# Optimization experiments

Measured on AMD Instinct MI355X. Metric: run time of the kernel, lower is better.

Reference implementation:

```python
import jax, jax.numpy as jnp
import numpy as np


def conv2d(x, w, b, stride, pad):
    # x: NCHW, w: OIHW (torch layout)
    y = jax.lax.conv_general_dilated(
        x, w, (stride, stride), ((pad, pad), (pad, pad)),
        dimension_numbers=('NCHW', 'OIHW', 'NCHW'))
    return y + b[None, :, None, None]


def conv_transpose2d(x, w, b, stride, pad):
    # w: torch ConvTranspose2d layout [in, out, kH, kW]
    k = w.shape[2]
    w_t = jnp.flip(w, (2, 3)).transpose(1, 0, 2, 3)  # -> OIHW
    p = k - 1 - pad
    y = jax.lax.conv_general_dilated(
        x, w_t, (1, 1), ((p, p), (p, p)), lhs_dilation=(stride, stride),
        dimension_numbers=('NCHW', 'OIHW', 'NCHW'))
    return y + b[None, :, None, None]


def resblock(x, w1, b1, w2, b2):
    h = jax.nn.relu(x)
    h = conv2d(h, w1, b1, 1, 1)   # 3x3
    h = jax.nn.relu(h)
    h = conv2d(h, w2, b2, 1, 0)   # 1x1
    return x + h


def setup_inputs() -> dict:
    key = jax.random.key(0)
    ks = iter(jax.random.split(key, 32))
    K, D = 512, 256
    s = 0.05

    def rn(shape):
        return (jax.random.normal(next(ks), shape, dtype=jnp.float32) * s)

    inp = {
        'x': jax.random.uniform(next(ks), (32, 3, 128, 128), dtype=jnp.float32),
        'e_c1_w': rn((256, 3, 4, 4)),   'e_c1_b': jnp.zeros((256,), jnp.float32),
        'e_c2_w': rn((256, 256, 4, 4)), 'e_c2_b': jnp.zeros((256,), jnp.float32),
        'e_r1_w1': rn((256, 256, 3, 3)), 'e_r1_b1': jnp.zeros((256,), jnp.float32),
        'e_r1_w2': rn((256, 256, 1, 1)), 'e_r1_b2': jnp.zeros((256,), jnp.float32),
        'e_r2_w1': rn((256, 256, 3, 3)), 'e_r2_b1': jnp.zeros((256,), jnp.float32),
        'e_r2_w2': rn((256, 256, 1, 1)), 'e_r2_b2': jnp.zeros((256,), jnp.float32),
        'emb': jax.random.normal(next(ks), (K, D), dtype=jnp.float32) / K,
        'd_r1_w1': rn((256, 256, 3, 3)), 'd_r1_b1': jnp.zeros((256,), jnp.float32),
        'd_r1_w2': rn((256, 256, 1, 1)), 'd_r1_b2': jnp.zeros((256,), jnp.float32),
        'd_r2_w1': rn((256, 256, 3, 3)), 'd_r2_b1': jnp.zeros((256,), jnp.float32),
        'd_r2_w2': rn((256, 256, 1, 1)), 'd_r2_b2': jnp.zeros((256,), jnp.float32),
        'd_t1_w': rn((256, 256, 4, 4)), 'd_t1_b': jnp.zeros((256,), jnp.float32),
        'd_t2_w': rn((256, 3, 4, 4)),   'd_t2_b': jnp.zeros((3,), jnp.float32),
    }
    return inp


def reference(x, e_c1_w, e_c1_b, e_c2_w, e_c2_b,
              e_r1_w1, e_r1_b1, e_r1_w2, e_r1_b2,
              e_r2_w1, e_r2_b1, e_r2_w2, e_r2_b2,
              emb,
              d_r1_w1, d_r1_b1, d_r1_w2, d_r1_b2,
              d_r2_w1, d_r2_b1, d_r2_w2, d_r2_b2,
              d_t1_w, d_t1_b, d_t2_w, d_t2_b):
    # ---- encoder ----
    h = jax.nn.relu(conv2d(x, e_c1_w, e_c1_b, 2, 1))
    h = jax.nn.relu(conv2d(h, e_c2_w, e_c2_b, 2, 1))
    h = resblock(h, e_r1_w1, e_r1_b1, e_r1_w2, e_r1_b2)
    z_e_x = resblock(h, e_r2_w1, e_r2_b1, e_r2_w2, e_r2_b2)  # [B,256,h,w]

    # ---- VQ: fused squared-distance + argmin (same math as
    # sum((z - e)^2, -2).argmin(-1), without the (B,h,w,256,K) intermediate) ----
    z = z_e_x.transpose(0, 2, 3, 1)                      # [B,h,w,256]
    z2 = jnp.sum(z * z, axis=-1, keepdims=True)          # [B,h,w,1]
    e2 = jnp.sum(emb * emb, axis=-1)                     # [K]
    dists = z2 - 2.0 * jnp.einsum('bhwd,kd->bhwk', z, emb) + e2
    latents = jnp.argmin(dists, axis=-1)                 # [B,h,w] int

    # ---- decoder ----
    z_q = emb[latents]                                   # [B,h,w,256]
    z_q_x = z_q.transpose(0, 3, 1, 2)                    # [B,256,h,w]
    d = resblock(z_q_x, d_r1_w1, d_r1_b1, d_r1_w2, d_r1_b2)
    d = resblock(d, d_r2_w1, d_r2_b1, d_r2_w2, d_r2_b2)
    d = jax.nn.relu(conv_transpose2d(d, d_t1_w, d_t1_b, 2, 1))
    x_tilde = jax.nn.sigmoid(conv_transpose2d(d, d_t2_w, d_t2_b, 2, 1))
    return x_tilde, z_e_x, z_q_x
```

## Files before the change

kernel.cpp:

```cpp
#include <hip/hip_runtime.h>
#include <math.h>

using frag_ab = __attribute__((ext_vector_type(8))) short;
using f32x4   = __attribute__((ext_vector_type(4))) float;

__device__ __forceinline__ unsigned short f2b(float f) {
    unsigned u = __float_as_uint(f);
    u += 0x7fffu + ((u >> 16) & 1u);
    return (unsigned short)(u >> 16);
}
__device__ __forceinline__ void bf8_to_f(uint4 v, float* f) {
    const unsigned* p = (const unsigned*)&v;
    #pragma unroll
    for (int q = 0; q < 4; ++q) {
        unsigned u = p[q];
        f[2*q]   = __uint_as_float(u << 16);
        f[2*q+1] = __uint_as_float(u & 0xffff0000u);
    }
}
__device__ __forceinline__ void gload16(const void* g, void* l) {
    __builtin_amdgcn_global_load_lds(g, l, 16, 0, 0);
}

__global__ void k_wt(const float* __restrict__ in, unsigned short* __restrict__ out,
                     int total, int CO, int CI, int sO, int sI) {
    int i = blockIdx.x * 256 + threadIdx.x;
    if (i >= total) return;
    int ci = i % CI;
    int r  = i / CI;
    int co = r % CO;
    int tp = r / CO;
    out[i] = f2b(in[(size_t)co * sO + (size_t)ci * sI + tp]);
}
__global__ void k_wt16(const float* __restrict__ in, unsigned short* __restrict__ out,
                       int sO, int sI) {
    int i = blockIdx.x * 256 + threadIdx.x;
    int ci = i & 255, co = i >> 8;
    const float* p = in + (size_t)co * sO + (size_t)ci * sI;
    #pragma unroll
    for (int tp = 0; tp < 16; ++tp)
        out[tp * 65536 + i] = f2b(p[tp]);
}
__global__ void k_wt3(const float* p0, const float* p1, const float* p2, const float* p3,
                      unsigned short* o0, unsigned short* o1, unsigned short* o2,
                      unsigned short* o3) {
    int z = blockIdx.y;
    const float* in = (z == 0) ? p0 : (z == 1) ? p1 : (z == 2) ? p2 : p3;
    unsigned short* out = (z == 0) ? o0 : (z == 1) ? o1 : (z == 2) ? o2 : o3;
    int i = blockIdx.x * 256 + threadIdx.x;
    int ci = i & 255, co = i >> 8;
    const float* p = in + (size_t)co * 2304 + (size_t)ci * 9;
    #pragma unroll
    for (int tp = 0; tp < 9; ++tp)
        out[tp * 65536 + i] = f2b(p[tp]);
}
__global__ void k_wt1(const float* p0, const float* p1, const float* p2, const float* p3,
                      unsigned short* o0, unsigned short* o1, unsigned short* o2,
                      unsigned short* o3) {
    int z = blockIdx.y;
    const float* in = (z == 0) ? p0 : (z == 1) ? p1 : (z == 2) ? p2 : p3;
    unsigned short* out = (z == 0) ? o0 : (z == 1) ? o1 : (z == 2) ? o2 : o3;
    int i = blockIdx.x * 256 + threadIdx.x;
    int ci = i & 255, co = i >> 8;
    out[i] = f2b(in[co * 256 + ci]);
}
__global__ void k_embcast(const float* __restrict__ in, unsigned short* __restrict__ out) {
    int i = blockIdx.x * 256 + threadIdx.x;
    out[i] = f2b(in[i]);
}

__global__ void k_e2(const float* __restrict__ emb, float* __restrict__ e2,
                     float* __restrict__ zpad) {
    if (blockIdx.x == 2) { zpad[threadIdx.x] = 0.f; return; }
    int k = blockIdx.x * 256 + threadIdx.x;
    if (k < 512) {
        const float* r = emb + k * 256;
        float s = 0.f;
        #pragma unroll 8
        for (int d = 0; d < 256; ++d) s += r[d] * r[d];
        e2[k] = s;
    }
}

__global__ __launch_bounds__(256) void k_conv1(const float* __restrict__ x,
        const float* __restrict__ w, const float* __restrict__ bias,
        unsigned short* __restrict__ out) {
    int t = threadIdx.x;
    int y = blockIdx.x * 4 + (t >> 6);
    int xq = t & 63;
    int b = blockIdx.y;
    int co0 = blockIdx.z * 64;
    float patch[48];
    #pragma unroll
    for (int ci = 0; ci < 3; ++ci)
        #pragma unroll
        for (int ky = 0; ky < 4; ++ky)
            #pragma unroll
            for (int kx = 0; kx < 4; ++kx) {
                int sy = 2*y - 1 + ky, sx = 2*xq - 1 + kx;
                float v = 0.f;
                if ((unsigned)sy < 128u && (unsigned)sx < 128u)
                    v = x[((b*3 + ci)*128 + sy)*128 + sx];
                patch[(ci*4 + ky)*4 + kx] = v;
            }
    unsigned short* op = out + (((size_t)(b*64 + y)*64 + xq) << 8) + co0;
    for (int c8 = 0; c8 < 8; ++c8) {
        unsigned short u8[8];
        #pragma unroll
        for (int cc = 0; cc < 8; ++cc) {
            int co = co0 + c8*8 + cc;
            float a = bias[co];
            #pragma unroll
            for (int k = 0; k < 48; ++k) a = fmaf(w[co*48 + k], patch[k], a);
            u8[cc] = f2b(fmaxf(a, 0.f));
        }
        *(uint4*)(op + c8*8) = *(uint4*)u8;
    }
}

template<int MODE, bool RELU_OUT, bool RELU_B16>
__global__ __launch_bounds__(256) void k_cgemm(
        const unsigned short* __restrict__ A,
        const unsigned short* __restrict__ Wt,
        const float* __restrict__ bias,
        const float* __restrict__ skipF,
        const unsigned short* __restrict__ zpad,
        unsigned short* __restrict__ outB,
        float* __restrict__ outFn,
        float* __restrict__ outFc) {
    constexpr int NTAPS = (MODE==0) ? 16 : (MODE==1) ? 9 : (MODE==2) ? 1 : 4;
    constexpr int HIN   = (MODE==0) ? 64 : 32;
    constexpr bool ISCT   = (MODE==3);

    __shared__ __align__(16) unsigned short As[128*128];
    __shared__ __align__(16) unsigned short Bs[128*128];

    int t = threadIdx.x;
    int cob = blockIdx.x;
    int y0  = blockIdx.y * 4;
    int bz  = blockIdx.z;
    int b   = ISCT ? (bz >> 2) : bz;
    int par = ISCT ? (bz & 3) : 0;
    int psy = par >> 1, psx = par & 1;

    int scc = t & 15, sr0 = t >> 4;
    int sc2 = scc ^ (sr0 & 7);

    int wv = t >> 6, lane = t & 63;
    int mq = (wv >> 1) * 64, nq = (wv & 1) * 64;
    int lg = lane >> 4, lr = lane & 15;

    f32x4 acc[4][4];
    #pragma unroll
    for (int i = 0; i < 4; ++i)
        #pragma unroll
        for (int j = 0; j < 4; ++j) acc[i][j] = (f32x4){0.f,0.f,0.f,0.f};

    for (int tap = 0; tap < NTAPS; ++tap) {
        int tdy, tdx, wtap;
        if (MODE == 0)      { tdy = tap >> 2; tdx = tap & 3; wtap = tap; }
        else if (MODE == 1) { tdy = tap / 3;  tdx = tap % 3; wtap = tap; }
        else if (MODE == 2) { tdy = 0; tdx = 0; wtap = 0; }
        else { int jy = tap >> 1, jx = tap & 1;
               tdy = psy - jy; tdx = psx - jx;
               wtap = ((psy ? 0 : 1) + 2*jy) * 4 + ((psx ? 0 : 1) + 2*jx); }
        const unsigned short* wb = Wt + ((size_t)wtap << 16) + ((size_t)cob << 15);

        for (int half = 0; half < 2; ++half) {
            int kk0 = half * 128;
            __syncthreads();
            #pragma unroll
            for (int q = 0; q < 8; ++q) {
                int row = sr0 + 16*q;
                int soy = y0 + (row >> 5), sox = row & 31;
                int sy = (MODE == 0) ? (2*soy - 1 + tdy)
                       : (MODE == 1) ? (soy - 1 + tdy) : (soy + tdy);
                int sx = (MODE == 0) ? (2*sox - 1 + tdx)
                       : (MODE == 1) ? (sox - 1 + tdx) : (sox + tdx);
                bool val = ((unsigned)sy < (unsigned)HIN) && ((unsigned)sx < (unsigned)HIN);
                const unsigned short* asrc = val
                    ? A + ((((size_t)(b*HIN + sy))*HIN + sx) << 8) + kk0 + sc2*8
                    : zpad;
                gload16(asrc, (char*)As + q*4096 + t*16);
                gload16(wb + (((size_t)row) << 8) + kk0 + sc2*8,
                        (char*)Bs + q*4096 + t*16);
            }
            __syncthreads();
            #pragma unroll
            for (int ks = 0; ks < 4; ++ks) {
                int c = ks*4 + lg;
                frag_ab af[4], bf[4];
                #pragma unroll
                for (int i = 0; i < 4; ++i) {
                    int ar = mq + i*16 + lr;
                    af[i] = *(const frag_ab*)((const char*)As + ar*256 + ((c ^ (ar & 7)) << 4));
                    int br = nq + i*16 + lr;
                    bf[i] = *(const frag_ab*)((const char*)Bs + br*256 + ((c ^ (br & 7)) << 4));
                }
                #pragma unroll
                for (int i = 0; i < 4; ++i)
                    #pragma unroll
                    for (int j = 0; j < 4; ++j)
                        acc[i][j] = __builtin_amdgcn_mfma_f32_16x16x32_bf16(
                                        af[i], bf[j], acc[i][j], 0, 0, 0);
            }
        }
    }

    #pragma unroll
    for (int mf = 0; mf < 4; ++mf) {
        #pragma unroll
        for (int nf = 0; nf < 4; ++nf) {
            int co = cob*128 + nq + nf*16 + lr;
            float bb = bias[co];
            f32x4 v = acc[mf][nf];
            #pragma unroll
            for (int j = 0; j < 4; ++j) {
                int prow = mq + mf*16 + lg*4 + j;
                int oy = y0 + (prow >> 5);
                int ox = prow & 31;
                size_t pix;
                if (ISCT) pix = ((size_t)(b*64 + (2*oy + psy)))*64 + (2*ox + psx);
                else      pix = ((size_t)(b*32 + oy))*32 + ox;
                float xv = v[j] + bb;
                if (skipF) xv += skipF[pix*256 + co];
                if (RELU_OUT) xv = fmaxf(xv, 0.f);
                if (outB)  outB[pix*256 + co] = f2b(RELU_B16 ? fmaxf(xv, 0.f) : xv);
                if (outFn) outFn[pix*256 + co] = xv;
                if (outFc) outFc[(((size_t)b*256 + co) << 10) + oy*32 + ox] = xv;
            }
        }
    }
}

__global__ __launch_bounds__(256) void k_vqm(const unsigned short* __restrict__ zB,
        const unsigned short* __restrict__ eB,
        const float* __restrict__ e2, int* __restrict__ lat) {
    __shared__ __align__(16) unsigned short As[64*256];
    __shared__ __align__(16) unsigned short Bs[64*256];
    int t = threadIdx.x;
    int pos0 = blockIdx.x * 64;
    #pragma unroll
    for (int q = 0; q < 8; ++q) {
        int idx = q*256 + t;
        int row = idx >> 5, ch = idx & 31;
        uint4 v = *(const uint4*)(zB + (((size_t)(pos0 + row)) << 8) + ch*8);
        *(uint4*)((char*)As + row*512 + ((ch ^ (row & 7)) << 4)) = v;
    }
    int wv = t >> 6, lane = t & 63;
    int lg = lane >> 4, lr = lane & 15;
    int arow = wv*16 + lr;
    int aswz[8];
    #pragma unroll
    for (int kk = 0; kk < 8; ++kk)
        aswz[kk] = arow*512 + (((kk*4 + lg) ^ (arow & 7)) << 4);
    float minv[4] = {1e30f, 1e30f, 1e30f, 1e30f};
    int   mink[4] = {0, 0, 0, 0};
    for (int kc = 0; kc < 8; ++kc) {
        __syncthreads();
        #pragma unroll
        for (int q = 0; q < 8; ++q) {
            int idx = q*256 + t;
            int row = idx >> 5, ch = idx & 31;
            uint4 v = *(const uint4*)(eB + (((size_t)(kc*64 + row)) << 8) + ch*8);
            *(uint4*)((char*)Bs + row*512 + ((ch ^ (row & 7)) << 4)) = v;
        }
        __syncthreads();
        #pragma unroll
        for (int nt = 0; nt < 4; ++nt) {
            int brow = nt*16 + lr;
            f32x4 acc = (f32x4){0.f, 0.f, 0.f, 0.f};
            #pragma unroll
            for (int kk = 0; kk < 8; ++kk) {
                frag_ab a = *(const frag_ab*)((const char*)As + aswz[kk]);
                frag_ab b = *(const frag_ab*)((const char*)Bs
                              + brow*512 + (((kk*4 + lg) ^ (brow & 7)) << 4));
                acc = __builtin_amdgcn_mfma_f32_16x16x32_bf16(a, b, acc, 0, 0, 0);
            }
            int k = kc*64 + nt*16 + lr;
            float ee = e2[k];
            #pragma unroll
            for (int j = 0; j < 4; ++j) {
                float dist = ee - 2.f * acc[j];
                if (dist < minv[j]) { minv[j] = dist; mink[j] = k; }
            }
        }
    }
    #pragma unroll
    for (int s = 1; s < 16; s <<= 1) {
        #pragma unroll
        for (int j = 0; j < 4; ++j) {
            float ov = __shfl_xor(minv[j], s, 64);
            int   ok = __shfl_xor(mink[j], s, 64);
            if (ov < minv[j] || (ov == minv[j] && ok < mink[j])) {
                minv[j] = ov; mink[j] = ok;
            }
        }
    }
    if (lr == 0) {
        #pragma unroll
        for (int j = 0; j < 4; ++j)
            lat[pos0 + wv*16 + lg*4 + j] = mink[j];
    }
}

__global__ __launch_bounds__(256) void k_gather(const int* __restrict__ lat,
        const float* __restrict__ emb, float* __restrict__ zqc,
        unsigned short* __restrict__ zqB, float* __restrict__ zqF) {
    __shared__ int ll[32];
    int t = threadIdx.x, y = blockIdx.x, b = blockIdx.y;
    if (t < 32) ll[t] = lat[(b * 32 + y) * 32 + t];
    __syncthreads();
    #pragma unroll
    for (int i = 0; i < 32; ++i) {
        int l = i * 256 + t;
        int d = l >> 5, xx = l & 31;
        zqc[(((size_t)b*256 + d) << 10) + y*32 + xx] = emb[ll[xx]*256 + d];
    }
    int xx = t & 31, dg = t >> 5;
    const float* e = emb + ll[xx]*256 + dg*32;
    size_t off = ((((size_t)(b*32 + y)*32 + xx)) << 8) + dg*32;
    #pragma unroll
    for (int q = 0; q < 8; ++q) {
        float4 v = *(const float4*)(e + q*4);
        *(float4*)(zqF + off + q*4) = v;
        uint2 pk;
        pk.x = (unsigned)f2b(fmaxf(v.x, 0.f)) | ((unsigned)f2b(fmaxf(v.y, 0.f)) << 16);
        pk.y = (unsigned)f2b(fmaxf(v.z, 0.f)) | ((unsigned)f2b(fmaxf(v.w, 0.f)) << 16);
        *(uint2*)(zqB + off + q*4) = pk;
    }
}

__global__ __launch_bounds__(256) void k_convt2(const unsigned short* __restrict__ in,
        const unsigned short* __restrict__ Wt,
        const float* __restrict__ bias, float* __restrict__ out) {
    __shared__ __align__(16) unsigned short slab[4*66*32];
    __shared__ __align__(16) unsigned short wl[16*3*32];
    int t = threadIdx.x;
    int b = blockIdx.y;
    int oy0 = blockIdx.x * 4;
    int u0 = oy0 >> 1;
    int oyl = t >> 7, ox = t & 127;
    int sy = oyl & 1, sx = ox & 1;
    int v = ox >> 1;
    float acc0[3] = {0.f,0.f,0.f}, acc1[3] = {0.f,0.f,0.f};
    for (int kc = 0; kc < 8; ++kc) {
        __syncthreads();
        for (int i = t; i < 4*66*4; i += 256) {
            int g = i & 3; int cidx = i >> 2;
            int cc = cidx % 66, ri = cidx / 66;
            int iy = u0 - 1 + ri, ix = cc - 1;
            uint4 v4 = {0,0,0,0};
            if ((unsigned)iy < 64u && (unsigned)ix < 64u)
                v4 = *(const uint4*)(in + (((size_t)(b*64 + iy)*64 + ix) << 8)
                                        + kc*32 + g*8);
            *(uint4*)(&slab[(ri*66 + cc)*32 + g*8]) = v4;
        }
        for (int i = t; i < 1536; i += 256)
            wl[i] = Wt[(i >> 5) * 256 + kc*32 + (i & 31)];
        __syncthreads();
        #pragma unroll
        for (int jy = 0; jy < 2; ++jy) {
            int duy = sy - jy;
            int riA = 1 + duy;
            #pragma unroll
            for (int jx = 0; jx < 2; ++jx) {
                int dvx = sx - jx;
                int cc = v + dvx + 1;
                int wtap = ((sy ? 0 : 1) + 2*jy)*4 + ((sx ? 0 : 1) + 2*jx);
                const unsigned short* sA = &slab[(riA*66 + cc)*32];
                const unsigned short* sB = sA + 66*32;
                const unsigned short* wp = &wl[wtap*96];
                #pragma unroll
                for (int c8 = 0; c8 < 4; ++c8) {
                    float fA[8], fB[8], w0[8], w1[8], w2[8];
                    bf8_to_f(*(const uint4*)(sA + c8*8), fA);
                    bf8_to_f(*(const uint4*)(sB + c8*8), fB);
                    bf8_to_f(*(const uint4*)(wp + c8*8), w0);
                    bf8_to_f(*(const uint4*)(wp + 32 + c8*8), w1);
                    bf8_to_f(*(const uint4*)(wp + 64 + c8*8), w2);
                    #pragma unroll
                    for (int q = 0; q < 8; ++q) {
                        acc0[0] = fmaf(fA[q], w0[q], acc0[0]);
                        acc0[1] = fmaf(fA[q], w1[q], acc0[1]);
                        acc0[2] = fmaf(fA[q], w2[q], acc0[2]);
                        acc1[0] = fmaf(fB[q], w0[q], acc1[0]);
                        acc1[1] = fmaf(fB[q], w1[q], acc1[1]);
                        acc1[2] = fmaf(fB[q], w2[q], acc1[2]);
                    }
                }
            }
        }
    }
    #pragma unroll
    for (int co = 0; co < 3; ++co) {
        float b0 = acc0[co] + bias[co];
        float b1 = acc1[co] + bias[co];
        out[(((size_t)b*3 + co) << 14) + (oy0 + oyl)*128 + ox]     = 1.f/(1.f + __expf(-b0));
        out[(((size_t)b*3 + co) << 14) + (oy0 + oyl + 2)*128 + ox] = 1.f/(1.f + __expf(-b1));
    }
}

extern "C" void kernel_launch(void* const* d_in, const int* in_sizes, int n_in,
                              void* d_out, int out_size, void* d_ws, size_t ws_size,
                              hipStream_t stream) {
    const float* x     = (const float*)d_in[0];
    const float* ec1w  = (const float*)d_in[1];
    const float* ec1b  = (const float*)d_in[2];
    const float* ec2w  = (const float*)d_in[3];
    const float* ec2b  = (const float*)d_in[4];
    const float* er1w1 = (const float*)d_in[5];
    const float* er1b1 = (const float*)d_in[6];
    const float* er1w2 = (const float*)d_in[7];
    const float* er1b2 = (const float*)d_in[8];
    const float* er2w1 = (const float*)d_in[9];
    const float* er2b1 = (const float*)d_in[10];
    const float* er2w2 = (const float*)d_in[11];
    const float* er2b2 = (const float*)d_in[12];
    const float* emb   = (const float*)d_in[13];
    const float* dr1w1 = (const float*)d_in[14];
    const float* dr1b1 = (const float*)d_in[15];
    const float* dr1w2 = (const float*)d_in[16];
    const float* dr1b2 = (const float*)d_in[17];
    const float* dr2w1 = (const float*)d_in[18];
    const float* dr2b1 = (const float*)d_in[19];
    const float* dr2w2 = (const float*)d_in[20];
    const float* dr2b2 = (const float*)d_in[21];
    const float* dt1w  = (const float*)d_in[22];
    const float* dt1b  = (const float*)d_in[23];
    const float* dt2w  = (const float*)d_in[24];
    const float* dt2b  = (const float*)d_in[25];

    float* outp = (float*)d_out;
    float* xt = outp;
    float* ze = outp + 1572864;
    float* zq = ze + 8388608;

    char* ws = (char*)d_ws;
    unsigned short* h1B  = (unsigned short*)(ws);
    unsigned short* B0   = (unsigned short*)(ws + 67108864);
    unsigned short* B1   = (unsigned short*)(ws + 83886080);
    unsigned short* T3   = (unsigned short*)(ws + 100663296);
    float*          F0   = (float*)(ws + 117440512);
    float*          F1   = (float*)(ws + 150994944);
    unsigned short* WtC2 = (unsigned short*)(ws + 184549376);
    unsigned short* Wt31 = (unsigned short*)(ws + 186646528);
    unsigned short* Wt32 = (unsigned short*)(ws + 187826176);
    unsigned short* Wt33 = (unsigned short*)(ws + 189005824);
    unsigned short* Wt34 = (unsigned short*)(ws + 190185472);
    unsigned short* W11  = (unsigned short*)(ws + 191365120);
    unsigned short* W12  = (unsigned short*)(ws + 191496192);
    unsigned short* W13  = (unsigned short*)(ws + 191627264);
    unsigned short* W14  = (unsigned short*)(ws + 191758336);
    unsigned short* WtT1 = (unsigned short*)(ws + 191889408);
    unsigned short* WtT2 = (unsigned short*)(ws + 193986560);
    float*          e2v  = (float*)(ws + 194011136);
    int*            lat  = (int*)(ws + 194013184);
    unsigned short* embB = (unsigned short*)(ws + 194144256);
    float*          zpad = (float*)(ws + 194406400);

    k_e2<<<3, 256, 0, stream>>>(emb, e2v, zpad);
    k_embcast<<<512, 256, 0, stream>>>(emb, embB);
    k_wt16<<<256, 256, 0, stream>>>(ec2w, WtC2, 4096, 16);
    k_wt16<<<256, 256, 0, stream>>>(dt1w, WtT1, 16, 4096);
    k_wt3<<<dim3(256, 4), 256, 0, stream>>>(er1w1, er2w1, dr1w1, dr2w1,
                                            Wt31, Wt32, Wt33, Wt34);
    k_wt1<<<dim3(256, 4), 256, 0, stream>>>(er1w2, er2w2, dr1w2, dr2w2,
                                            W11, W12, W13, W14);
    k_wt<<<48, 256, 0, stream>>>(dt2w, WtT2, 12288, 3, 256, 16, 48);

    const unsigned short* zp16 = (const unsigned short*)zpad;
    k_conv1<<<dim3(16, 32, 4), 256, 0, stream>>>(x, ec1w, ec1b, h1B);
    k_cgemm<0,true,false><<<dim3(2,8,32), 256, 0, stream>>>(h1B, WtC2, ec2b,
            nullptr, zp16, B0, F0, nullptr);
    k_cgemm<1,true,false><<<dim3(2,8,32), 256, 0, stream>>>(B0, Wt31, er1b1,
            nullptr, zp16, T3, nullptr, nullptr);
    k_cgemm<2,false,true><<<dim3(2,8,32), 256, 0, stream>>>(T3, W11, er1b2,
            F0, zp16, B1, F1, nullptr);
    k_cgemm<1,true,false><<<dim3(2,8,32), 256, 0, stream>>>(B1, Wt32, er2b1,
            nullptr, zp16, T3, nullptr, nullptr);
    k_cgemm<2,false,false><<<dim3(2,8,32), 256, 0, stream>>>(T3, W12, er2b2,
            F1, zp16, B0, nullptr, ze);
    k_vqm<<<512, 256, 0, stream>>>(B0, embB, e2v, lat);
    k_gather<<<dim3(32,32), 256, 0, stream>>>(lat, emb, zq, B0, F0);
    k_cgemm<1,true,false><<<dim3(2,8,32), 256, 0, stream>>>(B0, Wt33, dr1b1,
            nullptr, zp16, T3, nullptr, nullptr);
    k_cgemm<2,false,true><<<dim3(2,8,32), 256, 0, stream>>>(T3, W13, dr1b2,
            F0, zp16, B1, F1, nullptr);
    k_cgemm<1,true,false><<<dim3(2,8,32), 256, 0, stream>>>(B1, Wt34, dr2b1,
            nullptr, zp16, T3, nullptr, nullptr);
    k_cgemm<2,false,false><<<dim3(2,8,32), 256, 0, stream>>>(T3, W14, dr2b2,
            F1, zp16, B0, nullptr, nullptr);
    k_cgemm<3,true,false><<<dim3(2,8,128), 256, 0, stream>>>(B0, WtT1, dt1b,
            nullptr, zp16, h1B, nullptr, nullptr);
    k_convt2<<<dim3(32,32), 256, 0, stream>>>(h1B, WtT2, dt2b, xt);
}
```

Measured before the change: 1.001 ms.

## Double-buffer conv GEMM LDS tiles and pad convt2 slab rows

The shared conv GEMM kernel now splits each tap's K=256 into four 64-wide chunks held in two LDS buffers. The global-to-LDS load for chunk n+1 is issued before the MFMA work on chunk n, so loads overlap compute and each chunk needs one barrier instead of two. LDS footprint per buffer halves, but the loop runs more iterations with less MFMA work per barrier. Separately, the final transposed-conv kernel pads its slab row stride from 32 to 40 elements to reduce LDS bank conflicts.

New measurement: 964.6 us. 1.04x faster.

```diff
diff --git a/kernel.cpp b/kernel.cpp
--- a/kernel.cpp
+++ b/kernel.cpp
@@ -129,11 +129,12 @@
         float* __restrict__ outFn,
         float* __restrict__ outFc) {
     constexpr int NTAPS = (MODE==0) ? 16 : (MODE==1) ? 9 : (MODE==2) ? 1 : 4;
+    constexpr int NCH   = NTAPS * 4;
     constexpr int HIN   = (MODE==0) ? 64 : 32;
-    constexpr bool ISCT   = (MODE==3);
-
-    __shared__ __align__(16) unsigned short As[128*128];
-    __shared__ __align__(16) unsigned short Bs[128*128];
+    constexpr bool ISCT = (MODE==3);
+
+    __shared__ __align__(16) unsigned short As[2][128*64];
+    __shared__ __align__(16) unsigned short Bs[2][128*64];
 
     int t = threadIdx.x;
     int cob = blockIdx.x;
@@ -143,8 +144,9 @@
     int par = ISCT ? (bz & 3) : 0;
     int psy = par >> 1, psx = par & 1;
 
-    int scc = t & 15, sr0 = t >> 4;
-    int sc2 = scc ^ (sr0 & 7);
+    int srow = t >> 3;
+    int scc  = t & 7;
+    int sc2  = scc ^ (srow & 7);
 
     int wv = t >> 6, lane = t & 63;
     int mq = (wv >> 1) * 64, nq = (wv & 1) * 64;
@@ -156,7 +158,8 @@
         #pragma unroll
         for (int j = 0; j < 4; ++j) acc[i][j] = (f32x4){0.f,0.f,0.f,0.f};
 
-    for (int tap = 0; tap < NTAPS; ++tap) {
+    auto stage = [&](int n, int buf) {
+        int tap = n >> 2, kk0 = (n & 3) * 64;
         int tdy, tdx, wtap;
         if (MODE == 0)      { tdy = tap >> 2; tdx = tap & 3; wtap = tap; }
         else if (MODE == 1) { tdy = tap / 3;  tdx = tap % 3; wtap = tap; }
@@ -165,46 +168,48 @@
                tdy = psy - jy; tdx = psx - jx;
                wtap = ((psy ? 0 : 1) + 2*jy) * 4 + ((psx ? 0 : 1) + 2*jx); }
         const unsigned short* wb = Wt + ((size_t)wtap << 16) + ((size_t)cob << 15);
-
-        for (int half = 0; half < 2; ++half) {
-            int kk0 = half * 128;
-            __syncthreads();
-            #pragma unroll
-            for (int q = 0; q < 8; ++q) {
-                int row = sr0 + 16*q;
-                int soy = y0 + (row >> 5), sox = row & 31;
-                int sy = (MODE == 0) ? (2*soy - 1 + tdy)
-                       : (MODE == 1) ? (soy - 1 + tdy) : (soy + tdy);
-                int sx = (MODE == 0) ? (2*sox - 1 + tdx)
-                       : (MODE == 1) ? (sox - 1 + tdx) : (sox + tdx);
-                bool val = ((unsigned)sy < (unsigned)HIN) && ((unsigned)sx < (unsigned)HIN);
-                const unsigned short* asrc = val
-                    ? A + ((((size_t)(b*HIN + sy))*HIN + sx) << 8) + kk0 + sc2*8
-                    : zpad;
-                gload16(asrc, (char*)As + q*4096 + t*16);
-                gload16(wb + (((size_t)row) << 8) + kk0 + sc2*8,
-                        (char*)Bs + q*4096 + t*16);
-            }
-            __syncthreads();
-            #pragma unroll
-            for (int ks = 0; ks < 4; ++ks) {
-                int c = ks*4 + lg;
-                frag_ab af[4], bf[4];
+        #pragma unroll
+        for (int q = 0; q < 4; ++q) {
+            int row = srow + 32*q;
+            int soy = y0 + (row >> 5), sox = row & 31;
+            int sy = (MODE == 0) ? (2*soy - 1 + tdy)
+                   : (MODE == 1) ? (soy - 1 + tdy) : (soy + tdy);
+            int sx = (MODE == 0) ? (2*sox - 1 + tdx)
+                   : (MODE == 1) ? (sox - 1 + tdx) : (sox + tdx);
+            bool val = ((unsigned)sy < (unsigned)HIN) && ((unsigned)sx < (unsigned)HIN);
+            const unsigned short* asrc = val
+                ? A + ((((size_t)(b*HIN + sy))*HIN + sx) << 8) + kk0 + sc2*8
+                : zpad;
+            gload16(asrc, (char*)As[buf] + q*4096 + t*16);
+            gload16(wb + (((size_t)row) << 8) + kk0 + sc2*8,
+                    (char*)Bs[buf] + q*4096 + t*16);
+        }
+    };
+
+    stage(0, 0);
+    __syncthreads();
+    for (int n = 0; n < NCH; ++n) {
+        int cur = n & 1;
+        if (n + 1 < NCH) stage(n + 1, cur ^ 1);
+        #pragma unroll
+        for (int ks = 0; ks < 2; ++ks) {
+            int c = ks*4 + lg;
+            frag_ab af[4], bf[4];
+            #pragma unroll
+            for (int i = 0; i < 4; ++i) {
+                int ar = mq + i*16 + lr;
+                af[i] = *(const frag_ab*)((const char*)As[cur] + ar*128 + ((c ^ (ar & 7)) << 4));
+                int br = nq + i*16 + lr;
+                bf[i] = *(const frag_ab*)((const char*)Bs[cur] + br*128 + ((c ^ (br & 7)) << 4));
+            }
+            #pragma unroll
+            for (int i = 0; i < 4; ++i)
                 #pragma unroll
-                for (int i = 0; i < 4; ++i) {
-                    int ar = mq + i*16 + lr;
-                    af[i] = *(const frag_ab*)((const char*)As + ar*256 + ((c ^ (ar & 7)) << 4));
-                    int br = nq + i*16 + lr;
-                    bf[i] = *(const frag_ab*)((const char*)Bs + br*256 + ((c ^ (br & 7)) << 4));
-                }
-                #pragma unroll
-                for (int i = 0; i < 4; ++i)
-                    #pragma unroll
-                    for (int j = 0; j < 4; ++j)
-                        acc[i][j] = __builtin_amdgcn_mfma_f32_16x16x32_bf16(
-                                        af[i], bf[j], acc[i][j], 0, 0, 0);
-            }
-        }
+                for (int j = 0; j < 4; ++j)
+                    acc[i][j] = __builtin_amdgcn_mfma_f32_16x16x32_bf16(
+                                    af[i], bf[j], acc[i][j], 0, 0, 0);
+        }
+        __syncthreads();
     }
 
     #pragma unroll
@@ -334,7 +339,7 @@
 __global__ __launch_bounds__(256) void k_convt2(const unsigned short* __restrict__ in,
         const unsigned short* __restrict__ Wt,
         const float* __restrict__ bias, float* __restrict__ out) {
-    __shared__ __align__(16) unsigned short slab[4*66*32];
+    __shared__ __align__(16) unsigned short slab[4*66*40];
     __shared__ __align__(16) unsigned short wl[16*3*32];
     int t = threadIdx.x;
     int b = blockIdx.y;
@@ -354,7 +359,7 @@
             if ((unsigned)iy < 64u && (unsigned)ix < 64u)
                 v4 = *(const uint4*)(in + (((size_t)(b*64 + iy)*64 + ix) << 8)
                                         + kc*32 + g*8);
-            *(uint4*)(&slab[(ri*66 + cc)*32 + g*8]) = v4;
+            *(uint4*)(&slab[(ri*66 + cc)*40 + g*8]) = v4;
         }
         for (int i = t; i < 1536; i += 256)
             wl[i] = Wt[(i >> 5) * 256 + kc*32 + (i & 31)];
@@ -368,8 +373,8 @@
                 int dvx = sx - jx;
                 int cc = v + dvx + 1;
                 int wtap = ((sy ? 0 : 1) + 2*jy)*4 + ((sx ? 0 : 1) + 2*jx);
-                const unsigned short* sA = &slab[(riA*66 + cc)*32];
-                const unsigned short* sB = sA + 66*32;
+                const unsigned short* sA = &slab[(riA*66 + cc)*40];
+                const unsigned short* sB = sA + 66*40;
                 const unsigned short* wp = &wl[wtap*96];
                 #pragma unroll
                 for (int c8 = 0; c8 < 4; ++c8) {
```
